# Kernel tuning notes

Hardware: AMD Instinct MI355X
Metric: run time of the kernel (lower is better)

The kernel has to match this reference:

```python
import jax, jax.numpy as jnp
import numpy as np

B, S, D, H = 2, 2048, 1024, 16
HD = D // H                 # head_dim = 64
BLOCK = 16                  # _DEFAULT_BLOCK_SIZE
NB = S // BLOCK             # max_blocks_per_seq = 128
WINDOW = 512
NEG = jnp.float32(-1e30)


def setup_inputs() -> dict:
    key = jax.random.key(0)
    ks = jax.random.split(key, 5)
    x = jax.random.normal(ks[0], (B, S, D), jnp.float32)
    scale = D ** -0.5
    wq = jax.random.normal(ks[1], (D, D), jnp.float32) * scale
    wk = jax.random.normal(ks[2], (D, D), jnp.float32) * scale
    wv = jax.random.normal(ks[3], (D, D), jnp.float32) * scale
    wo = jax.random.normal(ks[4], (D, D), jnp.float32) * scale
    # sequential paged layout (matches the module's synthesized-cache fallback)
    block_tables = jnp.arange(B * NB, dtype=jnp.int32).reshape(B, NB)
    slot_mapping = jnp.arange(B * S, dtype=jnp.int32)
    context_lens = jnp.full((B,), S, dtype=jnp.int32)
    return {"x": x, "wq": wq, "wk": wk, "wv": wv, "wo": wo,
            "block_tables": block_tables, "slot_mapping": slot_mapping,
            "context_lens": context_lens, "window_size": WINDOW}


def reference(x, wq, wk, wv, wo, block_tables, slot_mapping, context_lens, window_size):
    b, s, d = x.shape
    # Q/K/V projections (nn.Linear, bias=False: y = x @ W^T)
    q = (x @ wq.T).reshape(b, s, H, HD)
    k = (x @ wk.T).reshape(b, s, H, HD)
    v = (x @ wv.T).reshape(b, s, H, HD)

    # ---- memopt_C.write_cache: scatter K/V into the physical slot pool ----
    num_slots = b * s
    key_cache = jnp.zeros((num_slots, H, HD), x.dtype).at[slot_mapping].set(k.reshape(-1, H, HD))
    value_cache = jnp.zeros((num_slots, H, HD), x.dtype).at[slot_mapping].set(v.reshape(-1, H, HD))

    # ---- dynamic_sparse_attention: read KV through block_tables ----
    t = jnp.arange(s)
    # physical slot of logical token t of sequence b: block_tables[b, t//BLOCK]*BLOCK + t%BLOCK
    slots = block_tables[:, t // BLOCK].astype(jnp.int32) * BLOCK + (t % BLOCK)[None, :].astype(jnp.int32)  # [B,S]
    kc = key_cache[slots]    # [B,S,H,HD]
    vc = value_cache[slots]  # [B,S,H,HD]

    scores = jnp.einsum('bqhd,bkhd->bhqk', q, kc) * (HD ** -0.5)  # [B,H,S,S]
    qpos = t[:, None]
    kpos = t[None, :]
    # causal + window-limited visibility (window_size tokens of history)
    vis = (kpos <= qpos) & (qpos - kpos < window_size)            # [S,S]
    ctx = t[None, :] < context_lens[:, None]                       # [B,S]
    mask = vis[None, None, :, :] & ctx[:, None, None, :]
    scores = jnp.where(mask, scores, NEG)
    attn = jax.nn.softmax(scores, axis=-1)
    out = jnp.einsum('bhqk,bkhd->bqhd', attn, vc).reshape(b, s, d)
    return out @ wo.T
```

## Files before the change

kernel.cpp:

```cpp
#include <hip/hip_runtime.h>

typedef __attribute__((ext_vector_type(4))) float  f32x4;
typedef __attribute__((ext_vector_type(8))) short  bf16x8;

typedef __attribute__((address_space(3))) void lds_void_t;
typedef __attribute__((address_space(1))) void g_void_t;

#define S_LEN  2048
#define DMODEL 1024
#define NHEAD  16
#define HDIM   64
#define NBLK   128
#define BATCH  2
#define KT     64
#define VP     72

__device__ __forceinline__ short f2bf(float f) {
  union { float f; unsigned u; } v; v.f = f;
  unsigned r = v.u + 0x7fffu + ((v.u >> 16) & 1u);
  return (short)(r >> 16);
}

__global__ __launch_bounds__(256) void cvt_all_kernel(
    const float* __restrict__ x,  const float* __restrict__ wq,
    const float* __restrict__ wk, const float* __restrict__ wv,
    const float* __restrict__ wo,
    short* __restrict__ xb,  short* __restrict__ wqb,
    short* __restrict__ wkb, short* __restrict__ wvb,
    short* __restrict__ wob) {
  const long i = ((long)blockIdx.x * 256 + threadIdx.x) * 8;
  const float* s; short* d; long off;
  if (i < 4194304L)      { s = x;  d = xb;  off = i; }
  else if (i < 5242880L) { s = wq; d = wqb; off = i - 4194304L; }
  else if (i < 6291456L) { s = wk; d = wkb; off = i - 5242880L; }
  else if (i < 7340032L) { s = wv; d = wvb; off = i - 6291456L; }
  else                   { s = wo; d = wob; off = i - 7340032L; }
  f32x4 a = *(const f32x4*)(s + off);
  f32x4 b = *(const f32x4*)(s + off + 4);
  bf16x8 o;
  o[0]=f2bf(a[0]); o[1]=f2bf(a[1]); o[2]=f2bf(a[2]); o[3]=f2bf(a[3]);
  o[4]=f2bf(b[0]); o[5]=f2bf(b[1]); o[6]=f2bf(b[2]); o[7]=f2bf(b[3]);
  *(bf16x8*)(d + off) = o;
}

__global__ __launch_bounds__(512, 2) void gemm8_kernel(
    const short* __restrict__ A,
    const short* __restrict__ W0, const short* __restrict__ W1, const short* __restrict__ W2,
    const int* __restrict__ slot_map,
    short* __restrict__ qbuf, short* __restrict__ kcache, short* __restrict__ vcache)
{
  extern __shared__ short smem[];

  const int m0 = blockIdx.x * 256;
  const int n0 = blockIdx.y * 192;
  const short* Ag = A + (size_t)m0 * DMODEL;

  const int tid  = threadIdx.x;
  const int wave = tid >> 6, lane = tid & 63;
  const int l15 = lane & 15, lg = lane >> 4;
  const int wr = wave >> 2, wc = wave & 3;
  const int swz = l15 & 7;

  short* const A0s = smem;
  short* const B0s = smem + 16384;
  short* const A1s = smem + 28672;
  short* const B1s = smem + 45056;

  f32x4 acc[8][3];
#pragma unroll
  for (int m = 0; m < 8; m++)
#pragma unroll
    for (int n = 0; n < 3; n++) acc[m][n] = (f32x4)0.f;

#define STAGE_A(DST, K0, P) {                                                              \
    const int gidx = (P) * 512 + tid;                                                      \
    const int r = gidx >> 3;                                                               \
    const int cs = (gidx & 7) ^ (r & 7);                                                   \
    __builtin_amdgcn_global_load_lds((g_void_t*)(Ag + (size_t)r * DMODEL + (K0) + cs * 8), \
        (lds_void_t*)((DST) + ((P) * 512 + wave * 64) * 8), 16, 0, 0); }

#define STAGE_B(DST, K0, P) {                                                              \
    const int gidx = (P) * 512 + tid;                                                      \
    const int r = gidx >> 3;                                                               \
    const int grow = n0 + r;                                                               \
    const short* wb = (grow < 1024) ? W0 : (grow < 2048) ? W1 : W2;                        \
    const int cs = (gidx & 7) ^ (r & 7);                                                   \
    __builtin_amdgcn_global_load_lds((g_void_t*)(wb + (size_t)(grow & 1023) * DMODEL + (K0) + cs * 8), \
        (lds_void_t*)((DST) + ((P) * 512 + wave * 64) * 8), 16, 0, 0); }

#define PHASE_BAR() do {                                        \
    asm volatile("" ::: "memory");                              \
    __builtin_amdgcn_s_barrier();                               \
    asm volatile("" ::: "memory");                              \
  } while (0)

#define PHASE_READ_A(BUF, Q)                                                               \
    _Pragma("unroll") for (int mi = 0; mi < 2; ++mi) {                                     \
      const int row = wr * 128 + ((Q) * 2 + mi) * 16 + l15;                                \
      _Pragma("unroll") for (int ks = 0; ks < 2; ++ks)                                     \
        af[mi][ks] = *(const bf16x8*)((BUF) + row * 64 + (((ks * 4 + lg) ^ swz) << 3)); }

#define PHASE_MFMA(Q)                                                                      \
    __builtin_amdgcn_s_setprio(1);                                                         \
    _Pragma("unroll") for (int mi = 0; mi < 2; ++mi)                                       \
    _Pragma("unroll") for (int nt = 0; nt < 3; ++nt)                                       \
    _Pragma("unroll") for (int ks = 0; ks < 2; ++ks)                                       \
      acc[(Q) * 2 + mi][nt] = __builtin_amdgcn_mfma_f32_16x16x32_bf16(                     \
          af[mi][ks], bfr[nt][ks], acc[(Q) * 2 + mi][nt], 0, 0, 0);                        \
    __builtin_amdgcn_s_setprio(0);

  STAGE_B(B0s, 0, 0); STAGE_B(B0s, 0, 1); STAGE_B(B0s, 0, 2);
  STAGE_A(A0s, 0, 0); STAGE_A(A0s, 0, 2); STAGE_A(A0s, 0, 1); STAGE_A(A0s, 0, 3);
  asm volatile("s_waitcnt vmcnt(0)" ::: "memory");
  __builtin_amdgcn_s_barrier();
  asm volatile("" ::: "memory");

  const int NT = DMODEL / 64;
  for (int t = 0; t < NT; ++t) {
    const bool stg = (t + 1 < NT);
    short* const Ac = (t & 1) ? A1s : A0s;
    short* const Bc = (t & 1) ? B1s : B0s;
    short* const An = (t & 1) ? A0s : A1s;
    short* const Bn = (t & 1) ? B0s : B1s;
    const int kn = (t + 1) * 64;

    bf16x8 af[2][2], bfr[3][2];

#pragma unroll
    for (int nt = 0; nt < 3; ++nt) {
      const int row = wc * 48 + nt * 16 + l15;
#pragma unroll
      for (int ks = 0; ks < 2; ++ks)
        bfr[nt][ks] = *(const bf16x8*)(Bc + row * 64 + (((ks * 4 + lg) ^ swz) << 3));
    }
    PHASE_READ_A(Ac, 0);
    if (stg) { STAGE_B(Bn, kn, 0); STAGE_B(Bn, kn, 1); STAGE_B(Bn, kn, 2); }
    PHASE_BAR();
    PHASE_MFMA(0);
    PHASE_BAR();

    PHASE_READ_A(Ac, 1);
    if (stg) { STAGE_A(An, kn, 0); STAGE_A(An, kn, 2); }
    PHASE_BAR();
    PHASE_MFMA(1);
    if (stg) { asm volatile("s_waitcnt vmcnt(5)" ::: "memory"); }
    else     { asm volatile("s_waitcnt vmcnt(0)" ::: "memory"); }
    PHASE_BAR();

    PHASE_READ_A(Ac, 2);
    if (stg) { STAGE_A(An, kn, 1); STAGE_A(An, kn, 3); }
    PHASE_BAR();
    PHASE_MFMA(2);
    PHASE_BAR();

    PHASE_READ_A(Ac, 3);
    PHASE_BAR();
    PHASE_MFMA(3);
    if (stg) { asm volatile("s_waitcnt vmcnt(2)" ::: "memory"); }
    else     { asm volatile("s_waitcnt vmcnt(0)" ::: "memory"); }
    PHASE_BAR();
  }
#undef STAGE_A
#undef STAGE_B
#undef PHASE_BAR
#undef PHASE_READ_A
#undef PHASE_MFMA

#pragma unroll
  for (int mf = 0; mf < 8; ++mf) {
    const int rowb = m0 + wr * 128 + mf * 16 + lg * 4;
#pragma unroll
    for (int r4 = 0; r4 < 4; ++r4) {
      const int row = rowb + r4;
      const int slot = slot_map[row];
#pragma unroll
      for (int nt = 0; nt < 3; ++nt) {
        const int col = n0 + wc * 48 + nt * 16 + l15;
        const short bv = f2bf(acc[mf][nt][r4]);
        if (col < DMODEL)
          qbuf[(size_t)row * DMODEL + col] = bv;
        else if (col < 2 * DMODEL)
          kcache[(size_t)slot * DMODEL + (col - DMODEL)] = bv;
        else
          vcache[(size_t)slot * DMODEL + (col - 2 * DMODEL)] = bv;
      }
    }
  }
}

__global__ __launch_bounds__(256, 2) void gemm1_kernel(
    const short* __restrict__ A, const short* __restrict__ W,
    float* __restrict__ outf)
{
  extern __shared__ short smem1[];

  const int m0 = blockIdx.x * 128;
  const int n0 = blockIdx.y * 128;
  const short* Ag = A + (size_t)m0 * DMODEL;
  const short* Bg = W + (size_t)n0 * DMODEL;

  const int tid = threadIdx.x;
  const int wave = tid >> 6, lane = tid & 63;
  const int l15 = lane & 15, lg = lane >> 4;
  const int wr = wave >> 1, wc = wave & 1;
  const int swz = l15 & 7;

  short* const As0 = smem1;
  short* const Bs0 = smem1 + 8192;
  short* const As1 = smem1 + 16384;
  short* const Bs1 = smem1 + 24576;

  f32x4 acc[4][4];
#pragma unroll
  for (int m = 0; m < 4; m++)
#pragma unroll
    for (int n = 0; n < 4; n++) acc[m][n] = (f32x4)0.f;

#define STG1(LA, LB, K0) {                                                                 \
    _Pragma("unroll") for (int p = 0; p < 4; ++p) {                                        \
      const int u = p * 256 + tid; const int r = u >> 3; const int cs = (u & 7) ^ (r & 7); \
      __builtin_amdgcn_global_load_lds((g_void_t*)(Ag + (size_t)r * DMODEL + (K0) + cs * 8), \
          (lds_void_t*)((LA) + (p * 256 + wave * 64) * 8), 16, 0, 0); }                    \
    _Pragma("unroll") for (int p = 0; p < 4; ++p) {                                        \
      const int u = p * 256 + tid; const int r = u >> 3; const int cs = (u & 7) ^ (r & 7); \
      __builtin_amdgcn_global_load_lds((g_void_t*)(Bg + (size_t)r * DMODEL + (K0) + cs * 8), \
          (lds_void_t*)((LB) + (p * 256 + wave * 64) * 8), 16, 0, 0); } }

  STG1(As0, Bs0, 0);
  asm volatile("s_waitcnt vmcnt(0)" ::: "memory");
  __builtin_amdgcn_s_barrier();
  asm volatile("" ::: "memory");

  for (int t = 0; t < 16; ++t) {
    const int cur = t & 1;
    short* const Ac = cur ? As1 : As0;
    short* const Bc = cur ? Bs1 : Bs0;
    short* const An = cur ? As0 : As1;
    short* const Bn = cur ? Bs0 : Bs1;
    if (t + 1 < 16) {
      STG1(An, Bn, (t + 1) * 64);
      asm volatile("s_waitcnt vmcnt(8)" ::: "memory");
    } else {
      asm volatile("s_waitcnt vmcnt(0)" ::: "memory");
    }
    asm volatile("" ::: "memory");
    __builtin_amdgcn_s_barrier();
    asm volatile("" ::: "memory");

    bf16x8 af[4][2], bfr[4][2];
#pragma unroll
    for (int m4 = 0; m4 < 4; ++m4) {
      const int row = wr * 64 + m4 * 16 + l15;
#pragma unroll
      for (int ks = 0; ks < 2; ++ks)
        af[m4][ks] = *(const bf16x8*)(Ac + row * 64 + (((ks * 4 + lg) ^ swz) << 3));
    }
#pragma unroll
    for (int n4 = 0; n4 < 4; ++n4) {
      const int row = wc * 64 + n4 * 16 + l15;
#pragma unroll
      for (int ks = 0; ks < 2; ++ks)
        bfr[n4][ks] = *(const bf16x8*)(Bc + row * 64 + (((ks * 4 + lg) ^ swz) << 3));
    }
    __builtin_amdgcn_s_setprio(1);
#pragma unroll
    for (int m4 = 0; m4 < 4; ++m4)
#pragma unroll
      for (int n4 = 0; n4 < 4; ++n4)
#pragma unroll
        for (int ks = 0; ks < 2; ++ks)
          acc[m4][n4] = __builtin_amdgcn_mfma_f32_16x16x32_bf16(af[m4][ks], bfr[n4][ks], acc[m4][n4], 0, 0, 0);
    __builtin_amdgcn_s_setprio(0);

    asm volatile("" ::: "memory");
    __builtin_amdgcn_s_barrier();
    asm volatile("" ::: "memory");
  }
#undef STG1

#pragma unroll
  for (int m4 = 0; m4 < 4; ++m4) {
    const int rowb = m0 + wr * 64 + m4 * 16 + lg * 4;
#pragma unroll
    for (int n4 = 0; n4 < 4; ++n4) {
      const int col = n0 + wc * 64 + n4 * 16 + l15;
#pragma unroll
      for (int r4 = 0; r4 < 4; ++r4)
        outf[(size_t)(rowb + r4) * DMODEL + col] = acc[m4][n4][r4];
    }
  }
}

__global__ __launch_bounds__(512, 4) void attn_kernel(
    const short* __restrict__ qbuf,
    const short* __restrict__ kcache, const short* __restrict__ vcache,
    const int* __restrict__ block_tables, const int* __restrict__ context_lens,
    const int* __restrict__ window_size,
    short* __restrict__ attn_out)
{
  __shared__ short Ks[KT * 64];
  __shared__ short Vt[HDIM * VP];
  __shared__ short Pb[8 * 16 * VP];

  const int b = blockIdx.z, h = blockIdx.y;
  const int bx = (b & 1) ? ((int)gridDim.x - 1 - (int)blockIdx.x) : (int)blockIdx.x;
  const int q0 = bx * 128;
  const int ctx = context_lens[b];
  const int ws  = window_size[0];
  const int* bt = block_tables + b * NBLK;

  const int tid  = threadIdx.x;
  const int wave = tid >> 6, lane = tid & 63;
  const int l15 = lane & 15, lg = lane >> 4;
  const int qw = q0 + wave * 16;

  const short* qp = qbuf + ((size_t)(b * S_LEN + qw + l15)) * DMODEL + h * HDIM;
  const bf16x8 qf0 = *(const bf16x8*)(qp + lg * 8);
  const bf16x8 qf1 = *(const bf16x8*)(qp + 32 + lg * 8);

  f32x4 oacc[4];
  float lrow[4];
#pragma unroll
  for (int i = 0; i < 4; i++) { oacc[i] = (f32x4)0.f; lrow[i] = 0.f; }

  int kstart = q0 - ws + 1; if (kstart < 0) kstart = 0; kstart &= ~(KT - 1);
  int kend = q0 + 128; if (kend > ctx) kend = ctx;

  const int kr = tid >> 3;
  const int dc = (tid & 7) << 3;
  const float rscale = 0.125f;
  const float FM = 12.f;
  short* pw = Pb + wave * (16 * VP);
  const int swz = (l15 & 7) << 4;

  bf16x8 kreg = (bf16x8)0, vreg = (bf16x8)0;
  {
    const int key = kstart + kr;
    if (key < ctx) {
      const int slot = bt[key >> 4] * 16 + (key & 15);
      kreg = *(const bf16x8*)(kcache + (size_t)slot * DMODEL + h * HDIM + dc);
      vreg = *(const bf16x8*)(vcache + (size_t)slot * DMODEL + h * HDIM + dc);
    }
  }

  for (int kt = kstart; kt < kend; kt += KT) {
    __syncthreads();
    *(bf16x8*)((char*)Ks + kr * 128 + ((dc * 2) ^ ((kr & 7) << 4))) = kreg;
    const int vcol = (kr + dc) & 63;
#pragma unroll
    for (int j = 0; j < 8; j++) Vt[(dc + j) * VP + vcol] = vreg[j];
    kreg = (bf16x8)0; vreg = (bf16x8)0;
    if (kt + KT < kend) {
      const int key = kt + KT + kr;
      if (key < ctx) {
        const int slot = bt[key >> 4] * 16 + (key & 15);
        kreg = *(const bf16x8*)(kcache + (size_t)slot * DMODEL + h * HDIM + dc);
        vreg = *(const bf16x8*)(vcache + (size_t)slot * DMODEL + h * HDIM + dc);
      }
    }
    __syncthreads();

    if ((kt > qw + 15) || (kt + (KT - 1) <= qw - ws)) continue;

    f32x4 sacc[4];
#pragma unroll
    for (int cg = 0; cg < 4; cg++) sacc[cg] = (f32x4)0.f;
#pragma unroll
    for (int cg = 0; cg < 4; cg++) {
      const char* kp = (const char*)Ks + (cg * 16 + l15) * 128;
      const bf16x8 k0 = *(const bf16x8*)(kp + ((lg * 16) ^ swz));
      const bf16x8 k1 = *(const bf16x8*)(kp + ((64 + lg * 16) ^ swz));
      sacc[cg] = __builtin_amdgcn_mfma_f32_16x16x32_bf16(qf0, k0, sacc[cg], 0, 0, 0);
      sacc[cg] = __builtin_amdgcn_mfma_f32_16x16x32_bf16(qf1, k1, sacc[cg], 0, 0, 0);
    }

    const bool fullvis = (kt + (KT - 1) <= qw) && (qw + 15 - kt < ws) && (kt + (KT - 1) < ctx);

    if (fullvis) {
#pragma unroll
      for (int r = 0; r < 4; r++) {
        const float e0 = __expf(sacc[0][r] * rscale - FM);
        const float e1 = __expf(sacc[1][r] * rscale - FM);
        const float e2 = __expf(sacc[2][r] * rscale - FM);
        const float e3 = __expf(sacc[3][r] * rscale - FM);
        lrow[r] += (e0 + e1) + (e2 + e3);
        short* pr = pw + (lg * 4 + r) * VP + l15;
        pr[0]  = f2bf(e0); pr[16] = f2bf(e1);
        pr[32] = f2bf(e2); pr[48] = f2bf(e3);
      }
    } else {
#pragma unroll
      for (int r = 0; r < 4; r++) {
        const int qrow = qw + lg * 4 + r;
        const int key0 = kt + l15;
        const bool ok0 = (key0      <= qrow) && (qrow - key0      < ws) && (key0      < ctx);
        const bool ok1 = (key0 + 16 <= qrow) && (qrow - key0 - 16 < ws) && (key0 + 16 < ctx);
        const bool ok2 = (key0 + 32 <= qrow) && (qrow - key0 - 32 < ws) && (key0 + 32 < ctx);
        const bool ok3 = (key0 + 48 <= qrow) && (qrow - key0 - 48 < ws) && (key0 + 48 < ctx);
        const float e0 = ok0 ? __expf(sacc[0][r] * rscale - FM) : 0.f;
        const float e1 = ok1 ? __expf(sacc[1][r] * rscale - FM) : 0.f;
        const float e2 = ok2 ? __expf(sacc[2][r] * rscale - FM) : 0.f;
        const float e3 = ok3 ? __expf(sacc[3][r] * rscale - FM) : 0.f;
        lrow[r] += (e0 + e1) + (e2 + e3);
        short* pr = pw + (lg * 4 + r) * VP + l15;
        pr[0]  = f2bf(e0); pr[16] = f2bf(e1);
        pr[32] = f2bf(e2); pr[48] = f2bf(e3);
      }
    }

    asm volatile("s_waitcnt lgkmcnt(0)" ::: "memory");

#pragma unroll
    for (int kk = 0; kk < 2; kk++) {
      const bf16x8 pa = *(const bf16x8*)(pw + l15 * VP + kk * 32 + lg * 8);
#pragma unroll
      for (int dn = 0; dn < 4; dn++) {
        const int vrow = dn * 16 + l15;
        const int roff = (kk * 32 + lg * 8 + (vrow & ~7)) & 63;
        const bf16x8 vb = *(const bf16x8*)(Vt + vrow * VP + roff);
        oacc[dn] = __builtin_amdgcn_mfma_f32_16x16x32_bf16(pa, vb, oacc[dn], 0, 0, 0);
      }
    }
  }

#pragma unroll
  for (int r = 0; r < 4; r++) {
    float ls = lrow[r];
    ls += __shfl_xor(ls, 1); ls += __shfl_xor(ls, 2);
    ls += __shfl_xor(ls, 4); ls += __shfl_xor(ls, 8);
    const float inv = 1.f / fmaxf(ls, 1e-30f);
    const int row = qw + lg * 4 + r;
    short* op = attn_out + ((size_t)(b * S_LEN + row)) * DMODEL + h * HDIM;
#pragma unroll
    for (int dn = 0; dn < 4; dn++)
      op[dn * 16 + l15] = f2bf(oacc[dn][r] * inv);
  }
}

extern "C" void kernel_launch(void* const* d_in, const int* in_sizes, int n_in,
                              void* d_out, int out_size, void* d_ws, size_t ws_size,
                              hipStream_t stream) {
  const float* x  = (const float*)d_in[0];
  const float* wq = (const float*)d_in[1];
  const float* wk = (const float*)d_in[2];
  const float* wv = (const float*)d_in[3];
  const float* wo = (const float*)d_in[4];
  const int* block_tables = (const int*)d_in[5];
  const int* slot_mapping = (const int*)d_in[6];
  const int* context_lens = (const int*)d_in[7];
  const int* window_size  = (const int*)d_in[8];
  float* out = (float*)d_out;

  char* ws = (char*)d_ws;
  short* xb     = (short*)(ws + (size_t)( 0 << 20));
  short* wqb    = (short*)(ws + (size_t)( 8 << 20));
  short* wkb    = (short*)(ws + (size_t)(10 << 20));
  short* wvb    = (short*)(ws + (size_t)(12 << 20));
  short* wob    = (short*)(ws + (size_t)(14 << 20));
  short* qbuf   = (short*)(ws + (size_t)(16 << 20));
  short* kcache = (short*)(ws + (size_t)(24 << 20));
  short* vcache = (short*)(ws + (size_t)(32 << 20));
  short* abuf   = (short*)(ws + (size_t)(40 << 20));

  static bool ginit = [] {
    hipFuncSetAttribute(reinterpret_cast<const void*>(&gemm8_kernel),
                        hipFuncAttributeMaxDynamicSharedMemorySize, 114688);
    hipFuncSetAttribute(reinterpret_cast<const void*>(&gemm1_kernel),
                        hipFuncAttributeMaxDynamicSharedMemorySize, 65536);
    return true;
  }();
  (void)ginit;

  cvt_all_kernel<<<4096, 256, 0, stream>>>(x, wq, wk, wv, wo, xb, wqb, wkb, wvb, wob);

  gemm8_kernel<<<dim3(16, 16), 512, 114688, stream>>>(xb, wqb, wkb, wvb, slot_mapping,
                                                      qbuf, kcache, vcache);

  attn_kernel<<<dim3(S_LEN / 128, NHEAD, BATCH), 512, 0, stream>>>(
      qbuf, kcache, vcache, block_tables, context_lens, window_size, abuf);

  gemm1_kernel<<<dim3(32, 8), 256, 65536, stream>>>(abuf, wob, out);
}
```

Baseline: 89.82 us.

## Halve QKV GEMM barrier phases and double-buffer attention K/V tiles

```diff
diff --git a/kernel.cpp b/kernel.cpp
--- a/kernel.cpp
+++ b/kernel.cpp
@@ -94,21 +94,6 @@
     asm volatile("" ::: "memory");                              \
   } while (0)
 
-#define PHASE_READ_A(BUF, Q)                                                               \
-    _Pragma("unroll") for (int mi = 0; mi < 2; ++mi) {                                     \
-      const int row = wr * 128 + ((Q) * 2 + mi) * 16 + l15;                                \
-      _Pragma("unroll") for (int ks = 0; ks < 2; ++ks)                                     \
-        af[mi][ks] = *(const bf16x8*)((BUF) + row * 64 + (((ks * 4 + lg) ^ swz) << 3)); }
-
-#define PHASE_MFMA(Q)                                                                      \
-    __builtin_amdgcn_s_setprio(1);                                                         \
-    _Pragma("unroll") for (int mi = 0; mi < 2; ++mi)                                       \
-    _Pragma("unroll") for (int nt = 0; nt < 3; ++nt)                                       \
-    _Pragma("unroll") for (int ks = 0; ks < 2; ++ks)                                       \
-      acc[(Q) * 2 + mi][nt] = __builtin_amdgcn_mfma_f32_16x16x32_bf16(                     \
-          af[mi][ks], bfr[nt][ks], acc[(Q) * 2 + mi][nt], 0, 0, 0);                        \
-    __builtin_amdgcn_s_setprio(0);
-
   STAGE_B(B0s, 0, 0); STAGE_B(B0s, 0, 1); STAGE_B(B0s, 0, 2);
   STAGE_A(A0s, 0, 0); STAGE_A(A0s, 0, 2); STAGE_A(A0s, 0, 1); STAGE_A(A0s, 0, 3);
   asm volatile("s_waitcnt vmcnt(0)" ::: "memory");
@@ -124,7 +109,7 @@
     short* const Bn = (t & 1) ? B0s : B1s;
     const int kn = (t + 1) * 64;
 
-    bf16x8 af[2][2], bfr[3][2];
+    bf16x8 af[4][2], bfr[3][2];
 
 #pragma unroll
     for (int nt = 0; nt < 3; ++nt) {
@@ -133,29 +118,49 @@
       for (int ks = 0; ks < 2; ++ks)
         bfr[nt][ks] = *(const bf16x8*)(Bc + row * 64 + (((ks * 4 + lg) ^ swz) << 3));
     }
-    PHASE_READ_A(Ac, 0);
-    if (stg) { STAGE_B(Bn, kn, 0); STAGE_B(Bn, kn, 1); STAGE_B(Bn, kn, 2); }
+#pragma unroll
+    for (int mi = 0; mi < 4; ++mi) {
+      const int row = wr * 128 + mi * 16 + l15;
+#pragma unroll
+      for (int ks = 0; ks < 2; ++ks)
+        af[mi][ks] = *(const bf16x8*)(Ac + row * 64 + (((ks * 4 + lg) ^ swz) << 3));
+    }
+    if (stg) { STAGE_B(Bn, kn, 0); STAGE_B(Bn, kn, 1); STAGE_B(Bn, kn, 2);
+               STAGE_A(An, kn, 0); STAGE_A(An, kn, 2); }
     PHASE_BAR();
-    PHASE_MFMA(0);
-    PHASE_BAR();
-
-    PHASE_READ_A(Ac, 1);
-    if (stg) { STAGE_A(An, kn, 0); STAGE_A(An, kn, 2); }
-    PHASE_BAR();
-    PHASE_MFMA(1);
+    __builtin_amdgcn_s_setprio(1);
+#pragma unroll
+    for (int mi = 0; mi < 4; ++mi)
+#pragma unroll
+      for (int nt = 0; nt < 3; ++nt)
+#pragma unroll
+        for (int ks = 0; ks < 2; ++ks)
+          acc[mi][nt] = __builtin_amdgcn_mfma_f32_16x16x32_bf16(
+              af[mi][ks], bfr[nt][ks], acc[mi][nt], 0, 0, 0);
+    __builtin_amdgcn_s_setprio(0);
     if (stg) { asm volatile("s_waitcnt vmcnt(5)" ::: "memory"); }
     else     { asm volatile("s_waitcnt vmcnt(0)" ::: "memory"); }
     PHASE_BAR();
 
-    PHASE_READ_A(Ac, 2);
+#pragma unroll
+    for (int mi = 0; mi < 4; ++mi) {
+      const int row = wr * 128 + 64 + mi * 16 + l15;
+#pragma unroll
+      for (int ks = 0; ks < 2; ++ks)
+        af[mi][ks] = *(const bf16x8*)(Ac + row * 64 + (((ks * 4 + lg) ^ swz) << 3));
+    }
     if (stg) { STAGE_A(An, kn, 1); STAGE_A(An, kn, 3); }
     PHASE_BAR();
-    PHASE_MFMA(2);
-    PHASE_BAR();
-
-    PHASE_READ_A(Ac, 3);
-    PHASE_BAR();
-    PHASE_MFMA(3);
+    __builtin_amdgcn_s_setprio(1);
+#pragma unroll
+    for (int mi = 0; mi < 4; ++mi)
+#pragma unroll
+      for (int nt = 0; nt < 3; ++nt)
+#pragma unroll
+        for (int ks = 0; ks < 2; ++ks)
+          acc[4 + mi][nt] = __builtin_amdgcn_mfma_f32_16x16x32_bf16(
+              af[mi][ks], bfr[nt][ks], acc[4 + mi][nt], 0, 0, 0);
+    __builtin_amdgcn_s_setprio(0);
     if (stg) { asm volatile("s_waitcnt vmcnt(2)" ::: "memory"); }
     else     { asm volatile("s_waitcnt vmcnt(0)" ::: "memory"); }
     PHASE_BAR();
@@ -163,8 +168,6 @@
 #undef STAGE_A
 #undef STAGE_B
 #undef PHASE_BAR
-#undef PHASE_READ_A
-#undef PHASE_MFMA
 
 #pragma unroll
   for (int mf = 0; mf < 8; ++mf) {
@@ -298,8 +301,8 @@
     const int* __restrict__ window_size,
     short* __restrict__ attn_out)
 {
-  __shared__ short Ks[KT * 64];
-  __shared__ short Vt[HDIM * VP];
+  __shared__ short Ks[2][KT * 64];
+  __shared__ short Vt[2][HDIM * VP];
   __shared__ short Pb[8 * 16 * VP];
 
   const int b = blockIdx.z, h = blockIdx.y;
@@ -343,12 +346,14 @@
     }
   }
 
-  for (int kt = kstart; kt < kend; kt += KT) {
-    __syncthreads();
-    *(bf16x8*)((char*)Ks + kr * 128 + ((dc * 2) ^ ((kr & 7) << 4))) = kreg;
+  int tix = 0;
+  for (int kt = kstart; kt < kend; kt += KT, ++tix) {
+    short* const KsB = Ks[tix & 1];
+    short* const VtB = Vt[tix & 1];
+    *(bf16x8*)((char*)KsB + kr * 128 + ((dc * 2) ^ ((kr & 7) << 4))) = kreg;
     const int vcol = (kr + dc) & 63;
 #pragma unroll
-    for (int j = 0; j < 8; j++) Vt[(dc + j) * VP + vcol] = vreg[j];
+    for (int j = 0; j < 8; j++) VtB[(dc + j) * VP + vcol] = vreg[j];
     kreg = (bf16x8)0; vreg = (bf16x8)0;
     if (kt + KT < kend) {
       const int key = kt + KT + kr;
@@ -367,7 +372,7 @@
     for (int cg = 0; cg < 4; cg++) sacc[cg] = (f32x4)0.f;
 #pragma unroll
     for (int cg = 0; cg < 4; cg++) {
-      const char* kp = (const char*)Ks + (cg * 16 + l15) * 128;
+      const char* kp = (const char*)KsB + (cg * 16 + l15) * 128;
       const bf16x8 k0 = *(const bf16x8*)(kp + ((lg * 16) ^ swz));
       const bf16x8 k1 = *(const bf16x8*)(kp + ((64 + lg * 16) ^ swz));
       sacc[cg] = __builtin_amdgcn_mfma_f32_16x16x32_bf16(qf0, k0, sacc[cg], 0, 0, 0);
@@ -417,7 +422,7 @@
       for (int dn = 0; dn < 4; dn++) {
         const int vrow = dn * 16 + l15;
         const int roff = (kk * 32 + lg * 8 + (vrow & ~7)) & 63;
-        const bf16x8 vb = *(const bf16x8*)(Vt + vrow * VP + roff);
+        const bf16x8 vb = *(const bf16x8*)(VtB + vrow * VP + roff);
         oacc[dn] = __builtin_amdgcn_mfma_f32_16x16x32_bf16(pa, vb, oacc[dn], 0, 0, 0);
       }
     }
```

After: 90.90 us. Within noise of the previous version (+1.2%).
